# Kernel tuning notes

Hardware: AMD Instinct MI355X
Metric: run time of the kernel (lower is better)

The kernel has to match this reference:

```python
import jax, jax.numpy as jnp
import numpy as np

N_HEADS = 4
HEAD_DIM = 64
N_EXPERTS = 64
TOP_K = 2
INPUT_DIM = 2048
N_TOKENS = 16384


def setup_inputs() -> dict:
    key = jax.random.key(0)
    ks = jax.random.split(key, 10)
    s = 0.02
    return {
        "x": jax.random.normal(ks[0], (N_TOKENS, INPUT_DIM), dtype=jnp.float32),
        "Wp": jax.random.normal(ks[1], (INPUT_DIM, N_HEADS * HEAD_DIM), dtype=jnp.float32) * s,
        "bp": jnp.zeros((N_HEADS * HEAD_DIM,), dtype=jnp.float32),
        "W1": jax.random.normal(ks[2], (N_HEADS, HEAD_DIM, HEAD_DIM), dtype=jnp.float32) * s,
        "b1": jnp.zeros((N_HEADS, HEAD_DIM), dtype=jnp.float32),
        "W2": jax.random.normal(ks[3], (N_HEADS, HEAD_DIM, N_EXPERTS), dtype=jnp.float32) * s,
        "b2": jnp.zeros((N_HEADS, N_EXPERTS), dtype=jnp.float32),
        "Wc": jax.random.normal(ks[4], (N_HEADS * N_EXPERTS, N_EXPERTS), dtype=jnp.float32) * s,
        "bc": jnp.zeros((N_EXPERTS,), dtype=jnp.float32),
        "temperature": jnp.ones((1,), dtype=jnp.float32) * 2.0,
        "noise_scale": jnp.ones((1,), dtype=jnp.float32) * 0.1,
    }


def reference(x, Wp, bp, W1, b1, W2, b2, Wc, bc, temperature, noise_scale):
    # eval-mode forward (no dropout, no routing noise)
    n = x.shape[0]
    h = (x @ Wp + bp).reshape(n, N_HEADS, HEAD_DIM)            # [N, 4, 64]
    hid = jax.nn.relu(jnp.einsum('nhd,hde->nhe', h, W1) + b1)   # [N, 4, 64]
    head_logits = jnp.einsum('nhd,hde->nhe', hid, W2) + b2      # [N, 4, E] (cat order = head order)
    combined = head_logits.reshape(n, N_HEADS * N_EXPERTS)      # [N, 4*E]
    gate_logits = combined @ Wc + bc                            # [N, E]
    gate_logits = gate_logits / jnp.clip(temperature, 0.5, 5.0)
    top_vals, top_idx = jax.lax.top_k(gate_logits, TOP_K)       # [N, k]
    top_gates = jax.nn.softmax(top_vals, axis=-1)
    gates = jnp.zeros_like(gate_logits).at[jnp.arange(n)[:, None], top_idx].set(top_gates)
    return gates, top_idx, gate_logits
```

## Files before the change

kernel.cpp:

```cpp
#include <hip/hip_runtime.h>
#include <math.h>

#define NT   16384
#define KD   2048
#define PROJ 256
#define NH   4
#define HD   64
#define NE   64

#define GATES_OFF 0
#define IDX_OFF   (NT * NE)
#define GL_OFF    (NT * NE + NT * 2)

typedef __attribute__((ext_vector_type(8))) short short8;
typedef __attribute__((ext_vector_type(4))) float f32x4;

static __device__ __forceinline__ ushort f2bf_rne(float f) {
    uint u = __float_as_uint(f);
    u += 0x7FFFu + ((u >> 16) & 1u);
    return (ushort)(u >> 16);
}
static __device__ __forceinline__ float bf2f(ushort b) {
    return __uint_as_float(((uint)b) << 16);
}

__global__ __launch_bounds__(256) void k0_split(const float* __restrict__ Wp,
                                                ushort* __restrict__ WpT_hi,
                                                ushort* __restrict__ WpT_lo)
{
    __shared__ ushort Th[64][72];
    __shared__ ushort Tl[64][72];

    const int t  = threadIdx.x;
    const int kb = blockIdx.x * 64;
    const int cb = blockIdx.y * 64;

#pragma unroll
    for (int q = 0; q < 4; ++q) {
        const int s   = t + q * 256;
        const int row = s >> 4;
        const int c4  = (s & 15) * 4;
        const float4 v = *(const float4*)&Wp[(size_t)(kb + row) * PROJ + cb + c4];
        const float vv[4] = { v.x, v.y, v.z, v.w };
#pragma unroll
        for (int j = 0; j < 4; ++j) {
            const ushort hi = f2bf_rne(vv[j]);
            const ushort lo = f2bf_rne(vv[j] - bf2f(hi));
            Th[c4 + j][row] = hi;
            Tl[c4 + j][row] = lo;
        }
    }
    __syncthreads();

#pragma unroll
    for (int q = 0; q < 2; ++q) {
        const int s    = t + q * 256;
        const int crow = s >> 3;
        const int kq   = (s & 7) * 8;
        *(uint4*)&WpT_hi[(size_t)(cb + crow) * KD + kb + kq] = *(const uint4*)&Th[crow][kq];
        *(uint4*)&WpT_lo[(size_t)(cb + crow) * KD + kb + kq] = *(const uint4*)&Tl[crow][kq];
    }
}

__global__ __launch_bounds__(256, 2) void k1_mfma(const float* __restrict__ x,
                                                  const ushort* __restrict__ WpT_hi,
                                                  const ushort* __restrict__ WpT_lo,
                                                  const float* __restrict__ bp,
                                                  float* __restrict__ hT)
{
    __shared__ ushort Ah[2][4096], Al[2][4096];

    const int t   = threadIdx.x;
    const int wid = t >> 6;
    const int wm4 = (wid >> 1) * 4;
    const int wn  = wid & 1;
    const int l   = t & 63;
    const int m0  = blockIdx.x * 128;
    const int n0  = blockIdx.y * 64;

    const int s0 = t, s1 = t + 256;
    const float* xa0 = &x[(size_t)(m0 + 16 * (s0 >> 6) + (s0 & 15)) * KD + ((s0 >> 4) & 3) * 8];
    const float* xa1 = &x[(size_t)(m0 + 16 * (s1 >> 6) + (s1 & 15)) * KD + ((s1 >> 4) & 3) * 8];

    const ushort* wph = &WpT_hi[(size_t)(n0 + wn * 32 + (l & 15)) * KD + (l >> 4) * 8];
    const ushort* wpl = &WpT_lo[(size_t)(n0 + wn * 32 + (l & 15)) * KD + (l >> 4) * 8];

    f32x4 acc[4][2];
#pragma unroll
    for (int m = 0; m < 4; ++m)
#pragma unroll
        for (int n = 0; n < 2; ++n) acc[m][n] = (f32x4){0.f, 0.f, 0.f, 0.f};

#define K1_STAGE_SLOT(DH, DL, VA, VB)                                          \
    {                                                                          \
        const float ff[8] = { (VA).x, (VA).y, (VA).z, (VA).w,                  \
                              (VB).x, (VB).y, (VB).z, (VB).w };                \
        uint hp[4], lp[4];                                                     \
        _Pragma("unroll")                                                      \
        for (int i = 0; i < 4; ++i) {                                          \
            const uint u0 = __float_as_uint(ff[2 * i]);                        \
            const uint u1 = __float_as_uint(ff[2 * i + 1]);                    \
            hp[i] = (u0 >> 16) | (u1 & 0xFFFF0000u);                           \
            const float r0 = ff[2 * i]     - __uint_as_float(u0 & 0xFFFF0000u);\
            const float r1 = ff[2 * i + 1] - __uint_as_float(u1 & 0xFFFF0000u);\
            lp[i] = (__float_as_uint(r0) >> 16) |                              \
                    (__float_as_uint(r1) & 0xFFFF0000u);                       \
        }                                                                      \
        *(uint4*)(DH) = (uint4){hp[0], hp[1], hp[2], hp[3]};                   \
        *(uint4*)(DL) = (uint4){lp[0], lp[1], lp[2], lp[3]};                   \
    }

#define K1_STAGE(BUF, R0, R1, R2, R3)                                          \
    K1_STAGE_SLOT(&Ah[BUF][s0 * 8], &Al[BUF][s0 * 8], R0, R1);                 \
    K1_STAGE_SLOT(&Ah[BUF][s1 * 8], &Al[BUF][s1 * 8], R2, R3);

#define K1_LOADA(KB, R0, R1, R2, R3)                                           \
    R0 = *(const float4*)(xa0 + (KB));                                         \
    R1 = *(const float4*)(xa0 + (KB) + 4);                                     \
    R2 = *(const float4*)(xa1 + (KB));                                         \
    R3 = *(const float4*)(xa1 + (KB) + 4);

#define K1_LOADB(KB, BH, BL)                                                   \
    _Pragma("unroll")                                                          \
    for (int n = 0; n < 2; ++n) {                                              \
        BH[n] = *(const short8*)(wph + (size_t)n * 16 * KD + (KB));            \
        BL[n] = *(const short8*)(wpl + (size_t)n * 16 * KD + (KB));            \
    }

#define K1_MFMA(BUF, BH, BL)                                                   \
    _Pragma("unroll")                                                          \
    for (int m = 0; m < 4; ++m) {                                              \
        const short8 ah = *(const short8*)&Ah[BUF][((wm4 + m) * 64 + l) * 8];  \
        const short8 al = *(const short8*)&Al[BUF][((wm4 + m) * 64 + l) * 8];  \
        _Pragma("unroll")                                                      \
        for (int n = 0; n < 2; ++n) {                                          \
            acc[m][n] = __builtin_amdgcn_mfma_f32_16x16x32_bf16(ah, BH[n], acc[m][n], 0, 0, 0); \
            acc[m][n] = __builtin_amdgcn_mfma_f32_16x16x32_bf16(ah, BL[n], acc[m][n], 0, 0, 0); \
            acc[m][n] = __builtin_amdgcn_mfma_f32_16x16x32_bf16(al, BH[n], acc[m][n], 0, 0, 0); \
        }                                                                      \
    }

    float4 xA0, xA1, xA2, xA3, xB0, xB1, xB2, xB3;
    short8 bhA[2], blA[2], bhB[2], blB[2];

    K1_LOADA(0, xA0, xA1, xA2, xA3);
    K1_LOADB(0, bhA, blA);

    for (int tp = 0; tp < 32; ++tp) {
        const int kb1 = (2 * tp + 1) * 32;
        const int kb2 = (2 * tp + 2) * 32;
        K1_STAGE(0, xA0, xA1, xA2, xA3);
        __syncthreads();
        K1_LOADA(kb1, xB0, xB1, xB2, xB3);
        K1_LOADB(kb1, bhB, blB);
        K1_MFMA(0, bhA, blA);
        K1_STAGE(1, xB0, xB1, xB2, xB3);
        __syncthreads();
        if (tp + 1 < 32) {
            K1_LOADA(kb2, xA0, xA1, xA2, xA3);
            K1_LOADB(kb2, bhA, blA);
        }
        K1_MFMA(1, bhB, blB);
    }

#pragma unroll
    for (int n = 0; n < 2; ++n) {
        const int col = n0 + wn * 32 + n * 16 + (l & 15);
        const float b = bp[col];
#pragma unroll
        for (int m = 0; m < 4; ++m) {
            const int tok = m0 + wm4 * 16 + m * 16 + (l >> 4) * 4;
            float4 st = { acc[m][n].x + b, acc[m][n].y + b,
                          acc[m][n].z + b, acc[m][n].w + b };
            *(float4*)&hT[(size_t)col * NT + tok] = st;
        }
    }
#undef K1_STAGE_SLOT
#undef K1_STAGE
#undef K1_LOADA
#undef K1_LOADB
#undef K1_MFMA
}

__global__ __launch_bounds__(256) void k2_heads(const float* __restrict__ hT,
                                                const float* __restrict__ W1,
                                                const float* __restrict__ b1,
                                                const float* __restrict__ W2,
                                                const float* __restrict__ b2,
                                                float* __restrict__ hlT)
{
    __shared__ float W1s[64][64];
    __shared__ float W2s[64][64];
    __shared__ float Hs[64][132];

    const int t    = threadIdx.x;
    const int eg   = t & 15;
    const int tg   = t >> 4;
    const int head = blockIdx.y;
    const int tok0 = blockIdx.x * 128;

    {
        const float4* g1 = (const float4*)(W1 + (size_t)head * HD * HD);
        const float4* g2 = (const float4*)(W2 + (size_t)head * HD * HD);
        float4* s1 = (float4*)&W1s[0][0];
        float4* s2 = (float4*)&W2s[0][0];
#pragma unroll
        for (int q = 0; q < 4; ++q) {
            s1[t + q * 256] = g1[t + q * 256];
            s2[t + q * 256] = g2[t + q * 256];
        }
    }
    const float4 b1v = *(const float4*)&b1[head * HD + eg * 4];
    const float4 b2v = *(const float4*)&b2[head * HD + eg * 4];
    __syncthreads();

    float acc[4][8];
    {
        const float bb[4] = { b1v.x, b1v.y, b1v.z, b1v.w };
#pragma unroll
        for (int j = 0; j < 4; ++j)
#pragma unroll
            for (int i = 0; i < 8; ++i) acc[j][i] = bb[j];
    }
    const float* hbase = &hT[(size_t)(head * HD) * NT + tok0 + tg * 8];
#pragma unroll 4
    for (int d = 0; d < HD; ++d) {
        const float4 w  = *(const float4*)&W1s[d][eg * 4];
        const float4 h0 = *(const float4*)&hbase[(size_t)d * NT];
        const float4 h1 = *(const float4*)&hbase[(size_t)d * NT + 4];
        const float wv[4] = { w.x, w.y, w.z, w.w };
        const float hv[8] = { h0.x, h0.y, h0.z, h0.w, h1.x, h1.y, h1.z, h1.w };
#pragma unroll
        for (int j = 0; j < 4; ++j)
#pragma unroll
            for (int i = 0; i < 8; ++i)
                acc[j][i] = fmaf(wv[j], hv[i], acc[j][i]);
    }
#pragma unroll
    for (int j = 0; j < 4; ++j) {
        float4 lo, hi;
        lo.x = fmaxf(acc[j][0], 0.f); lo.y = fmaxf(acc[j][1], 0.f);
        lo.z = fmaxf(acc[j][2], 0.f); lo.w = fmaxf(acc[j][3], 0.f);
        hi.x = fmaxf(acc[j][4], 0.f); hi.y = fmaxf(acc[j][5], 0.f);
        hi.z = fmaxf(acc[j][6], 0.f); hi.w = fmaxf(acc[j][7], 0.f);
        *(float4*)&Hs[eg * 4 + j][tg * 8]     = lo;
        *(float4*)&Hs[eg * 4 + j][tg * 8 + 4] = hi;
    }
    __syncthreads();

    {
        const float bb[4] = { b2v.x, b2v.y, b2v.z, b2v.w };
#pragma unroll
        for (int j = 0; j < 4; ++j)
#pragma unroll
            for (int i = 0; i < 8; ++i) acc[j][i] = bb[j];
    }
#pragma unroll 4
    for (int d = 0; d < HD; ++d) {
        const float4 w  = *(const float4*)&W2s[d][eg * 4];
        const float4 h0 = *(const float4*)&Hs[d][tg * 8];
        const float4 h1 = *(const float4*)&Hs[d][tg * 8 + 4];
        const float wv[4] = { w.x, w.y, w.z, w.w };
        const float hv[8] = { h0.x, h0.y, h0.z, h0.w, h1.x, h1.y, h1.z, h1.w };
#pragma unroll
        for (int j = 0; j < 4; ++j)
#pragma unroll
            for (int i = 0; i < 8; ++i)
                acc[j][i] = fmaf(wv[j], hv[i], acc[j][i]);
    }
#pragma unroll
    for (int j = 0; j < 4; ++j) {
        float4 lo = { acc[j][0], acc[j][1], acc[j][2], acc[j][3] };
        float4 hi = { acc[j][4], acc[j][5], acc[j][6], acc[j][7] };
        float* dst = &hlT[(size_t)(head * HD + eg * 4 + j) * NT + tok0 + tg * 8];
        *(float4*)&dst[0] = lo;
        *(float4*)&dst[4] = hi;
    }
}

__global__ __launch_bounds__(512) void k3_gate(const float* __restrict__ hlT,
                                               const float* __restrict__ Wc,
                                               const float* __restrict__ bc,
                                               const float* __restrict__ temp,
                                               float* __restrict__ out)
{
    const int t    = threadIdx.x;
    const int eg   = t & 15;
    const int tg   = t >> 4;
    const int tok0 = blockIdx.x * 64;

    const float tv  = fminf(fmaxf(temp[0], 0.5f), 5.0f);
    const float inv = 1.0f / tv;
    const float4 bcv = *(const float4*)&bc[eg * 4];

    float acc[4][2];
    acc[0][0] = bcv.x; acc[0][1] = bcv.x;
    acc[1][0] = bcv.y; acc[1][1] = bcv.y;
    acc[2][0] = bcv.z; acc[2][1] = bcv.z;
    acc[3][0] = bcv.w; acc[3][1] = bcv.w;

    const float* hb = &hlT[tok0 + tg * 2];
#pragma unroll 8
    for (int k = 0; k < PROJ; ++k) {
        const float2 hv = *(const float2*)&hb[(size_t)k * NT];
        const float4 wv = *(const float4*)&Wc[k * NE + eg * 4];
        const float wa[4] = { wv.x, wv.y, wv.z, wv.w };
#pragma unroll
        for (int j = 0; j < 4; ++j) {
            acc[j][0] = fmaf(wa[j], hv.x, acc[j][0]);
            acc[j][1] = fmaf(wa[j], hv.y, acc[j][1]);
        }
    }

#pragma unroll
    for (int i = 0; i < 2; ++i) {
        const int tok = tok0 + tg * 2 + i;
        float gl_[4];
#pragma unroll
        for (int j = 0; j < 4; ++j) gl_[j] = acc[j][i] * inv;

        float v1 = gl_[0]; int i1 = eg * 4;
#pragma unroll
        for (int j = 1; j < 4; ++j)
            if (gl_[j] > v1) { v1 = gl_[j]; i1 = eg * 4 + j; }
#pragma unroll
        for (int off = 8; off >= 1; off >>= 1) {
            const float ov = __shfl_xor(v1, off);
            const int   oi = __shfl_xor(i1, off);
            if (ov > v1 || (ov == v1 && oi < i1)) { v1 = ov; i1 = oi; }
        }
        float v2 = -INFINITY; int i2 = NE;
#pragma unroll
        for (int j = 0; j < 4; ++j) {
            const int e = eg * 4 + j;
            if (e != i1 && gl_[j] > v2) { v2 = gl_[j]; i2 = e; }
        }
#pragma unroll
        for (int off = 8; off >= 1; off >>= 1) {
            const float ov = __shfl_xor(v2, off);
            const int   oi = __shfl_xor(i2, off);
            if (ov > v2 || (ov == v2 && oi < i2)) { v2 = ov; i2 = oi; }
        }

        const float e2  = expf(v2 - v1);
        const float s   = 1.f + e2;
        const float g1v = 1.f / s;
        const float g2v = e2 / s;

        float4 gv;
        {
            const int e0 = eg * 4;
            gv.x = (e0 + 0 == i1) ? g1v : ((e0 + 0 == i2) ? g2v : 0.f);
            gv.y = (e0 + 1 == i1) ? g1v : ((e0 + 1 == i2) ? g2v : 0.f);
            gv.z = (e0 + 2 == i1) ? g1v : ((e0 + 2 == i2) ? g2v : 0.f);
            gv.w = (e0 + 3 == i1) ? g1v : ((e0 + 3 == i2) ? g2v : 0.f);
        }
        *(float4*)&out[GATES_OFF + (size_t)tok * NE + eg * 4] = gv;
        const float4 glv = { gl_[0], gl_[1], gl_[2], gl_[3] };
        *(float4*)&out[GL_OFF + (size_t)tok * NE + eg * 4] = glv;
        if (eg == 0) {
            out[IDX_OFF + (size_t)tok * 2 + 0] = (float)i1;
            out[IDX_OFF + (size_t)tok * 2 + 1] = (float)i2;
        }
    }
}

extern "C" void kernel_launch(void* const* d_in, const int* in_sizes, int n_in,
                              void* d_out, int out_size, void* d_ws, size_t ws_size,
                              hipStream_t stream)
{
    (void)in_sizes; (void)n_in; (void)out_size; (void)ws_size;

    const float* x    = (const float*)d_in[0];
    const float* Wp   = (const float*)d_in[1];
    const float* bp   = (const float*)d_in[2];
    const float* W1   = (const float*)d_in[3];
    const float* b1   = (const float*)d_in[4];
    const float* W2   = (const float*)d_in[5];
    const float* b2   = (const float*)d_in[6];
    const float* Wc   = (const float*)d_in[7];
    const float* bc   = (const float*)d_in[8];
    const float* temp = (const float*)d_in[9];

    float* out = (float*)d_out;
    float* hT  = (float*)d_ws;
    float* hlT = hT + (size_t)PROJ * NT;

    ushort* WpT_hi = (ushort*)hlT;
    ushort* WpT_lo = WpT_hi + (size_t)KD * PROJ;

    k0_split<<<dim3(KD / 64, PROJ / 64), 256, 0, stream>>>(Wp, WpT_hi, WpT_lo);
    k1_mfma <<<dim3(NT / 128, PROJ / 64), 256, 0, stream>>>(x, WpT_hi, WpT_lo, bp, hT);
    k2_heads<<<dim3(NT / 128, NH),        256, 0, stream>>>(hT, W1, b1, W2, b2, hlT);
    k3_gate <<<dim3(NT / 64),             512, 0, stream>>>(hlT, Wc, bc, temp, out);
}
```

Before: 219.5 us.

## Load x fragments directly into registers and drop LDS staging in projection GEMM

```diff
diff --git a/kernel.cpp b/kernel.cpp
--- a/kernel.cpp
+++ b/kernel.cpp
@@ -24,6 +24,27 @@
     return __uint_as_float(((uint)b) << 16);
 }
 
+static __device__ __forceinline__ void split8(const float4 a, const float4 b,
+                                              short8& hi8, short8& lo8)
+{
+    const float f[8] = { a.x, a.y, a.z, a.w, b.x, b.y, b.z, b.w };
+    uint hp[4], lp[4];
+#pragma unroll
+    for (int i = 0; i < 4; ++i) {
+        const uint u0 = __float_as_uint(f[2 * i]);
+        const uint u1 = __float_as_uint(f[2 * i + 1]);
+        hp[i] = __builtin_amdgcn_perm(u1, u0, 0x07060302u);
+        const float r0 = f[2 * i]     - __uint_as_float(u0 & 0xFFFF0000u);
+        const float r1 = f[2 * i + 1] - __uint_as_float(u1 & 0xFFFF0000u);
+        lp[i] = __builtin_amdgcn_perm(__float_as_uint(r1), __float_as_uint(r0),
+                                      0x07060302u);
+    }
+    const uint4 hv = { hp[0], hp[1], hp[2], hp[3] };
+    const uint4 lv = { lp[0], lp[1], lp[2], lp[3] };
+    hi8 = *(const short8*)&hv;
+    lo8 = *(const short8*)&lv;
+}
+
 __global__ __launch_bounds__(256) void k0_split(const float* __restrict__ Wp,
                                                 ushort* __restrict__ WpT_hi,
                                                 ushort* __restrict__ WpT_lo)
@@ -62,14 +83,12 @@
     }
 }
 
-__global__ __launch_bounds__(256, 2) void k1_mfma(const float* __restrict__ x,
-                                                  const ushort* __restrict__ WpT_hi,
-                                                  const ushort* __restrict__ WpT_lo,
-                                                  const float* __restrict__ bp,
-                                                  float* __restrict__ hT)
-{
-    __shared__ ushort Ah[2][4096], Al[2][4096];
-
+__global__ __launch_bounds__(256) void k1_mfma(const float* __restrict__ x,
+                                               const ushort* __restrict__ WpT_hi,
+                                               const ushort* __restrict__ WpT_lo,
+                                               const float* __restrict__ bp,
+                                               float* __restrict__ hT)
+{
     const int t   = threadIdx.x;
     const int wid = t >> 6;
     const int wm4 = (wid >> 1) * 4;
@@ -78,10 +97,7 @@
     const int m0  = blockIdx.x * 128;
     const int n0  = blockIdx.y * 64;
 
-    const int s0 = t, s1 = t + 256;
-    const float* xa0 = &x[(size_t)(m0 + 16 * (s0 >> 6) + (s0 & 15)) * KD + ((s0 >> 4) & 3) * 8];
-    const float* xa1 = &x[(size_t)(m0 + 16 * (s1 >> 6) + (s1 & 15)) * KD + ((s1 >> 4) & 3) * 8];
-
+    const float* xa = &x[(size_t)(m0 + wm4 * 16 + (l & 15)) * KD + (l >> 4) * 8];
     const ushort* wph = &WpT_hi[(size_t)(n0 + wn * 32 + (l & 15)) * KD + (l >> 4) * 8];
     const ushort* wpl = &WpT_lo[(size_t)(n0 + wn * 32 + (l & 15)) * KD + (l >> 4) * 8];
 
@@ -91,34 +107,12 @@
 #pragma unroll
         for (int n = 0; n < 2; ++n) acc[m][n] = (f32x4){0.f, 0.f, 0.f, 0.f};
 
-#define K1_STAGE_SLOT(DH, DL, VA, VB)                                          \
-    {                                                                          \
-        const float ff[8] = { (VA).x, (VA).y, (VA).z, (VA).w,                  \
-                              (VB).x, (VB).y, (VB).z, (VB).w };                \
-        uint hp[4], lp[4];                                                     \
-        _Pragma("unroll")                                                      \
-        for (int i = 0; i < 4; ++i) {                                          \
-            const uint u0 = __float_as_uint(ff[2 * i]);                        \
-            const uint u1 = __float_as_uint(ff[2 * i + 1]);                    \
-            hp[i] = (u0 >> 16) | (u1 & 0xFFFF0000u);                           \
-            const float r0 = ff[2 * i]     - __uint_as_float(u0 & 0xFFFF0000u);\
-            const float r1 = ff[2 * i + 1] - __uint_as_float(u1 & 0xFFFF0000u);\
-            lp[i] = (__float_as_uint(r0) >> 16) |                              \
-                    (__float_as_uint(r1) & 0xFFFF0000u);                       \
-        }                                                                      \
-        *(uint4*)(DH) = (uint4){hp[0], hp[1], hp[2], hp[3]};                   \
-        *(uint4*)(DL) = (uint4){lp[0], lp[1], lp[2], lp[3]};                   \
-    }
-
-#define K1_STAGE(BUF, R0, R1, R2, R3)                                          \
-    K1_STAGE_SLOT(&Ah[BUF][s0 * 8], &Al[BUF][s0 * 8], R0, R1);                 \
-    K1_STAGE_SLOT(&Ah[BUF][s1 * 8], &Al[BUF][s1 * 8], R2, R3);
-
-#define K1_LOADA(KB, R0, R1, R2, R3)                                           \
-    R0 = *(const float4*)(xa0 + (KB));                                         \
-    R1 = *(const float4*)(xa0 + (KB) + 4);                                     \
-    R2 = *(const float4*)(xa1 + (KB));                                         \
-    R3 = *(const float4*)(xa1 + (KB) + 4);
+#define K1_LOADA(KB, PA)                                                       \
+    _Pragma("unroll")                                                          \
+    for (int m = 0; m < 4; ++m) {                                              \
+        PA[m][0] = *(const float4*)(xa + (size_t)m * 16 * KD + (KB));          \
+        PA[m][1] = *(const float4*)(xa + (size_t)m * 16 * KD + (KB) + 4);      \
+    }
 
 #define K1_LOADB(KB, BH, BL)                                                   \
     _Pragma("unroll")                                                          \
@@ -127,11 +121,11 @@
         BL[n] = *(const short8*)(wpl + (size_t)n * 16 * KD + (KB));            \
     }
 
-#define K1_MFMA(BUF, BH, BL)                                                   \
+#define K1_COMPUTE(PA, BH, BL)                                                 \
     _Pragma("unroll")                                                          \
     for (int m = 0; m < 4; ++m) {                                              \
-        const short8 ah = *(const short8*)&Ah[BUF][((wm4 + m) * 64 + l) * 8];  \
-        const short8 al = *(const short8*)&Al[BUF][((wm4 + m) * 64 + l) * 8];  \
+        short8 ah, al;                                                         \
+        split8(PA[m][0], PA[m][1], ah, al);                                    \
         _Pragma("unroll")                                                      \
         for (int n = 0; n < 2; ++n) {                                          \
             acc[m][n] = __builtin_amdgcn_mfma_f32_16x16x32_bf16(ah, BH[n], acc[m][n], 0, 0, 0); \
@@ -140,27 +134,23 @@
         }                                                                      \
     }
 
-    float4 xA0, xA1, xA2, xA3, xB0, xB1, xB2, xB3;
+    float4 paA[4][2], paB[4][2];
     short8 bhA[2], blA[2], bhB[2], blB[2];
 
-    K1_LOADA(0, xA0, xA1, xA2, xA3);
+    K1_LOADA(0, paA);
     K1_LOADB(0, bhA, blA);
 
     for (int tp = 0; tp < 32; ++tp) {
         const int kb1 = (2 * tp + 1) * 32;
         const int kb2 = (2 * tp + 2) * 32;
-        K1_STAGE(0, xA0, xA1, xA2, xA3);
-        __syncthreads();
-        K1_LOADA(kb1, xB0, xB1, xB2, xB3);
+        K1_LOADA(kb1, paB);
         K1_LOADB(kb1, bhB, blB);
-        K1_MFMA(0, bhA, blA);
-        K1_STAGE(1, xB0, xB1, xB2, xB3);
-        __syncthreads();
+        K1_COMPUTE(paA, bhA, blA);
         if (tp + 1 < 32) {
-            K1_LOADA(kb2, xA0, xA1, xA2, xA3);
+            K1_LOADA(kb2, paA);
             K1_LOADB(kb2, bhA, blA);
         }
-        K1_MFMA(1, bhB, blB);
+        K1_COMPUTE(paB, bhB, blB);
     }
 
 #pragma unroll
@@ -175,11 +165,9 @@
             *(float4*)&hT[(size_t)col * NT + tok] = st;
         }
     }
-#undef K1_STAGE_SLOT
-#undef K1_STAGE
 #undef K1_LOADA
 #undef K1_LOADB
-#undef K1_MFMA
+#undef K1_COMPUTE
 }
 
 __global__ __launch_bounds__(256) void k2_heads(const float* __restrict__ hT,
```

New measurement: 276.3 us. 25.8% more time.

## Deepen x prefetch in projection GEMM and use LDS-only barriers

Applied to the files above, without the earlier changes.

```diff
diff --git a/kernel.cpp b/kernel.cpp
--- a/kernel.cpp
+++ b/kernel.cpp
@@ -22,6 +22,12 @@
 }
 static __device__ __forceinline__ float bf2f(ushort b) {
     return __uint_as_float(((uint)b) << 16);
+}
+
+static __device__ __forceinline__ void barrier_lds_only() {
+    asm volatile("s_waitcnt lgkmcnt(0)" ::: "memory");
+    __builtin_amdgcn_s_barrier();
+    asm volatile("" ::: "memory");
 }
 
 __global__ __launch_bounds__(256) void k0_split(const float* __restrict__ Wp,
@@ -110,15 +116,15 @@
         *(uint4*)(DL) = (uint4){lp[0], lp[1], lp[2], lp[3]};                   \
     }
 
-#define K1_STAGE(BUF, R0, R1, R2, R3)                                          \
-    K1_STAGE_SLOT(&Ah[BUF][s0 * 8], &Al[BUF][s0 * 8], R0, R1);                 \
-    K1_STAGE_SLOT(&Ah[BUF][s1 * 8], &Al[BUF][s1 * 8], R2, R3);
-
-#define K1_LOADA(KB, R0, R1, R2, R3)                                           \
-    R0 = *(const float4*)(xa0 + (KB));                                         \
-    R1 = *(const float4*)(xa0 + (KB) + 4);                                     \
-    R2 = *(const float4*)(xa1 + (KB));                                         \
-    R3 = *(const float4*)(xa1 + (KB) + 4);
+#define K1_STAGE(BUF, PA)                                                      \
+    K1_STAGE_SLOT(&Ah[BUF][s0 * 8], &Al[BUF][s0 * 8], PA[0], PA[1]);           \
+    K1_STAGE_SLOT(&Ah[BUF][s1 * 8], &Al[BUF][s1 * 8], PA[2], PA[3]);
+
+#define K1_LOADA(KB, PA)                                                       \
+    PA[0] = *(const float4*)(xa0 + (KB));                                      \
+    PA[1] = *(const float4*)(xa0 + (KB) + 4);                                  \
+    PA[2] = *(const float4*)(xa1 + (KB));                                      \
+    PA[3] = *(const float4*)(xa1 + (KB) + 4);
 
 #define K1_LOADB(KB, BH, BL)                                                   \
     _Pragma("unroll")                                                          \
@@ -140,27 +146,30 @@
         }                                                                      \
     }
 
-    float4 xA0, xA1, xA2, xA3, xB0, xB1, xB2, xB3;
-    short8 bhA[2], blA[2], bhB[2], blB[2];
-
-    K1_LOADA(0, xA0, xA1, xA2, xA3);
-    K1_LOADB(0, bhA, blA);
+    float4 A0[4], A1[4];
+    short8 bh0[2], bl0[2], bh1[2], bl1[2];
+
+    K1_LOADA(0, A0);
+    K1_LOADA(32, A1);
+    K1_LOADB(0, bh0, bl0);
+    K1_STAGE(0, A0);
+    K1_LOADA(2 * 32, A0);
+    barrier_lds_only();
 
     for (int tp = 0; tp < 32; ++tp) {
-        const int kb1 = (2 * tp + 1) * 32;
-        const int kb2 = (2 * tp + 2) * 32;
-        K1_STAGE(0, xA0, xA1, xA2, xA3);
-        __syncthreads();
-        K1_LOADA(kb1, xB0, xB1, xB2, xB3);
-        K1_LOADB(kb1, bhB, blB);
-        K1_MFMA(0, bhA, blA);
-        K1_STAGE(1, xB0, xB1, xB2, xB3);
-        __syncthreads();
-        if (tp + 1 < 32) {
-            K1_LOADA(kb2, xA0, xA1, xA2, xA3);
-            K1_LOADB(kb2, bhA, blA);
-        }
-        K1_MFMA(1, bhB, blB);
+        const int t1 = 2 * tp + 1;
+        K1_LOADB(t1 * 32, bh1, bl1);
+        K1_MFMA(0, bh0, bl0);
+        K1_STAGE(1, A1);
+        if (t1 + 2 < 64) { K1_LOADA((t1 + 2) * 32, A1); }
+        barrier_lds_only();
+        if (t1 + 1 < 64) { K1_LOADB((t1 + 1) * 32, bh0, bl0); }
+        K1_MFMA(1, bh1, bl1);
+        if (t1 + 1 < 64) {
+            K1_STAGE(0, A0);
+            if (t1 + 3 < 64) { K1_LOADA((t1 + 3) * 32, A0); }
+            barrier_lds_only();
+        }
     }
 
 #pragma unroll
```

Measured after the change: 218.9 us. About the same (-0.3%).
